# Kernel tuning notes

Hardware: AMD Instinct MI355X
Metric: run time of the kernel (lower is better)

The kernel has to match this reference:

```python
import jax, jax.numpy as jnp
import numpy as np

B, T, C, H = 2, 2048, 1024, 16
D = C // H
NEG = -1e9


def setup_inputs() -> dict:
    key = jax.random.key(0)
    ks = jax.random.split(key, 16)
    s = C ** -0.5
    hidden_states = jax.random.normal(ks[0], (B, T, C), dtype=jnp.float32)
    causal = jnp.tril(jnp.ones((T, T), dtype=bool))
    attention_mask = jnp.where(causal, 0.0, NEG).astype(jnp.float32)[None, None]
    p = lambda k, sh: jax.random.normal(k, sh, dtype=jnp.float32) * s
    return {
        "hidden_states": hidden_states,
        "attention_mask": attention_mask,
        "Wq": p(ks[1], (C, C)), "bq": jnp.zeros((C,), jnp.float32),
        "Wk": p(ks[2], (C, C)), "bk": jnp.zeros((C,), jnp.float32),
        "Wv": p(ks[3], (C, C)), "bv": jnp.zeros((C,), jnp.float32),
        "Wo": p(ks[4], (C, C)), "bo": jnp.zeros((C,), jnp.float32),
        "Wr1": p(ks[5], (C, C)), "br1": jnp.zeros((C,), jnp.float32),
        "Wr2": p(ks[6], (C, 3)), "br2": jnp.zeros((3,), jnp.float32),
    }


def reference(hidden_states, attention_mask, Wq, bq, Wk, bk, Wv, bv, Wo, bo, Wr1, br1, Wr2, br2):
    b, t, c = hidden_states.shape
    scale = D ** -0.5
    q = (hidden_states @ Wq + bq).reshape(b, t, H, D)
    k = (hidden_states @ Wk + bk).reshape(b, t, H, D)
    v = (hidden_states @ Wv + bv).reshape(b, t, H, D)
    # dead-end routing MLP (gate_logits computed but unused in the original)
    gate_logits = jnp.tanh(hidden_states @ Wr1 + br1) @ Wr2 + br2
    lambdas = jax.nn.softmax(gate_logits, axis=-1)  # noqa: F841 (unused, faithful)
    # explicit (unfused) attention: [B,H,T,T] scores materialized
    scores = jnp.einsum("bqhd,bkhd->bhqk", q, k) * scale + attention_mask
    probs = jax.nn.softmax(scores, axis=-1)
    ctx = jnp.einsum("bhqk,bkhd->bqhd", probs, v).reshape(b, t, c)
    return ctx @ Wo + bo
```

## Files before the change

### kernel.cpp

```cpp
#include <hip/hip_runtime.h>
#include <hip/hip_fp16.h>
#include <math.h>

#define BDIM 2
#define TDIM 2048
#define CDIM 1024
#define HDIM 16
#define DDIM 64

typedef _Float16 f16x8 __attribute__((ext_vector_type(8)));
typedef float f32x4 __attribute__((ext_vector_type(4)));

#define GLL16(gsrc, ldst)                                                      \
  __builtin_amdgcn_global_load_lds(                                            \
      (const __attribute__((address_space(1))) unsigned int*)(gsrc),           \
      (__attribute__((address_space(3))) unsigned int*)(ldst), 16, 0, 0)

#define SWZ(row) ((((row)&7) ^ (((row) >> 3) & 7)) << 4)

__global__ __launch_bounds__(256) void cvt_f16(const float* __restrict__ in,
                                               __half* __restrict__ out,
                                               int n8) {
  int i = blockIdx.x * blockDim.x + threadIdx.x;
  if (i >= n8) return;
  const float4* p = (const float4*)in + (size_t)i * 2;
  float4 a = p[0], b = p[1];
  __half2* o = (__half2*)out + (size_t)i * 4;
  o[0] = __floats2half2_rn(a.x, a.y);
  o[1] = __floats2half2_rn(a.z, a.w);
  o[2] = __floats2half2_rn(b.x, b.y);
  o[3] = __floats2half2_rn(b.z, b.w);
}

__global__ __launch_bounds__(256) void transpose_cvt(
    const float* __restrict__ w0, const float* __restrict__ w1,
    const float* __restrict__ w2, const float* __restrict__ w3,
    __half* __restrict__ o0, __half* __restrict__ o1, __half* __restrict__ o2,
    __half* __restrict__ o3) {
  const float* src;
  __half* dst;
  switch (blockIdx.z) {
    case 0: src = w0; dst = o0; break;
    case 1: src = w1; dst = o1; break;
    case 2: src = w2; dst = o2; break;
    default: src = w3; dst = o3; break;
  }
  __shared__ float t[32][33];
  const int tx = threadIdx.x & 31, ty = threadIdx.x >> 5;
  const int k0 = blockIdx.y * 32, n0 = blockIdx.x * 32;
#pragma unroll
  for (int j = 0; j < 4; ++j)
    t[ty + j * 8][tx] = src[(size_t)(k0 + ty + j * 8) * CDIM + n0 + tx];
  __syncthreads();
#pragma unroll
  for (int j = 0; j < 4; ++j)
    dst[(size_t)(n0 + ty + j * 8) * CDIM + k0 + tx] =
        __float2half(t[tx][ty + j * 8]);
}

template <int NMAT, int OUT16>
__global__ __launch_bounds__(256) void gemm_f16_bt(
    const __half* __restrict__ A, const __half* __restrict__ Bt,
    const float* __restrict__ bias0, const float* __restrict__ bias1,
    const float* __restrict__ bias2, float* __restrict__ outf,
    __half* __restrict__ outh, int M, int K) {
  __shared__ _Float16 As[2][128][32];
  __shared__ _Float16 Bs[2][128][32];
  const int tid = threadIdx.x;
  const int wid = tid >> 6, lane = tid & 63;
  const int m0 = blockIdx.y * 128, n0 = blockIdx.x * 128;
  const int wr = (wid >> 1) * 64, wc = (wid & 1) * 64;
  const int srow = lane >> 2;
  const int scol = (lane & 3) * 8;

  const __half* asrc = A + (size_t)(m0 + wid * 32 + srow) * K + scol;
  const __half* bsrc = Bt + (size_t)(n0 + wid * 32 + srow) * K + scol;

  f32x4 acc[4][4] = {};
  const int NT = K / 32;

  GLL16(asrc, &As[0][wid * 32][0]);
  GLL16(asrc + 16 * K, &As[0][wid * 32 + 16][0]);
  GLL16(bsrc, &Bs[0][wid * 32][0]);
  GLL16(bsrc + 16 * K, &Bs[0][wid * 32 + 16][0]);
  __syncthreads();

  for (int t = 0; t < NT; ++t) {
    const int cur = t & 1;
    if (t + 1 < NT) {
      const int k0 = (t + 1) * 32;
      GLL16(asrc + k0, &As[cur ^ 1][wid * 32][0]);
      GLL16(asrc + k0 + 16 * K, &As[cur ^ 1][wid * 32 + 16][0]);
      GLL16(bsrc + k0, &Bs[cur ^ 1][wid * 32][0]);
      GLL16(bsrc + k0 + 16 * K, &Bs[cur ^ 1][wid * 32 + 16][0]);
    }
    f16x8 a[4], b[4];
#pragma unroll
    for (int m = 0; m < 4; ++m)
      a[m] =
          *(const f16x8*)&As[cur][wr + m * 16 + (lane & 15)][(lane >> 4) * 8];
#pragma unroll
    for (int n = 0; n < 4; ++n)
      b[n] =
          *(const f16x8*)&Bs[cur][wc + n * 16 + (lane & 15)][(lane >> 4) * 8];
#pragma unroll
    for (int m = 0; m < 4; ++m)
#pragma unroll
      for (int n = 0; n < 4; ++n)
        acc[m][n] = __builtin_amdgcn_mfma_f32_16x16x32_f16(a[m], b[n],
                                                           acc[m][n], 0, 0, 0);
    __syncthreads();
  }

  const float* bias = bias0;
  size_t obase = 0;
  int ncol0 = n0;
  if (NMAT == 3) {
    const int mat = n0 >> 10;
    bias = (mat == 0) ? bias0 : (mat == 1) ? bias1 : bias2;
    obase = (size_t)mat * ((size_t)M * CDIM);
    ncol0 = n0 & 1023;
  }
#pragma unroll
  for (int m = 0; m < 4; ++m)
#pragma unroll
    for (int n = 0; n < 4; ++n) {
      const int col = ncol0 + wc + n * 16 + (lane & 15);
      const float bb = bias[col];
#pragma unroll
      for (int j = 0; j < 4; ++j) {
        const int row = m0 + wr + m * 16 + (lane >> 4) * 4 + j;
        if (OUT16)
          outh[obase + (size_t)row * CDIM + col] =
              __float2half(acc[m][n][j] + bb);
        else
          outf[(size_t)row * CDIM + col] = acc[m][n][j] + bb;
      }
    }
}

__global__ __launch_bounds__(256) void attention_mfma(
    const __half* __restrict__ q, const __half* __restrict__ k,
    const __half* __restrict__ v, __half* __restrict__ ctx) {
  __shared__ _Float16 Kl[2][64][64];
  __shared__ _Float16 Vt[2][64][64];
  __shared__ _Float16 Pl[4][16][64];

  const int tid = threadIdx.x;
  const int wid = tid >> 6, lane = tid & 63;
  const int qt = (blockIdx.x + blockIdx.y) & 31;
  const int bh = blockIdx.y;
  const int b = bh >> 4, h = bh & 15;
  const int qbase = qt * 64;
  const int g = lane >> 4, r = lane & 15;

  const __half* qhead = q + ((size_t)b * TDIM) * CDIM + h * DDIM;
  const __half* khead = k + ((size_t)b * TDIM) * CDIM + h * DDIM;
  const __half* vhead = v + ((size_t)b * TDIM) * CDIM + h * DDIM;

  f16x8 qf[2];
  {
    const __half* qrow = qhead + (size_t)(qbase + wid * 16 + r) * CDIM;
    qf[0] = *(const f16x8*)(qrow + g * 8);
    qf[1] = *(const f16x8*)(qrow + g * 8 + 32);
  }

  const int vrow = tid >> 2, vcol = (tid & 3) * 16;
  const int kr8 = lane >> 3;
  const int c0 = wid * 2, c1 = wid * 2 + 1;
  const int kcol0 = (((lane & 7) ^ kr8 ^ c0) & 7) * 8;
  const int kcol1 = (((lane & 7) ^ kr8 ^ c1) & 7) * 8;

  f32x4 acc_c[4] = {};
  float mj[4] = {-3.0e38f, -3.0e38f, -3.0e38f, -3.0e38f};
  float lj[4] = {};

  const int nt = qt + 1;

  f16x8 va, vb;
  {
    const __half* vsrc = vhead + (size_t)vrow * CDIM + vcol;
    va = *(const f16x8*)(vsrc);
    vb = *(const f16x8*)(vsrc + 8);
    GLL16(khead + (size_t)(c0 * 8 + kr8) * CDIM + kcol0, &Kl[0][c0 * 8][0]);
    GLL16(khead + (size_t)(c1 * 8 + kr8) * CDIM + kcol1, &Kl[0][c1 * 8][0]);
  }
  asm volatile("s_waitcnt vmcnt(0)" ::: "memory");
  __builtin_amdgcn_sched_barrier(0);
  {
    char* vt0 = (char*)&Vt[0][0][0];
#pragma unroll
    for (int i = 0; i < 8; ++i) {
      const int d0 = vcol + i, d1 = vcol + 8 + i;
      *(_Float16*)(vt0 + d0 * 128 + ((vrow * 2) ^ SWZ(d0))) = va[i];
      *(_Float16*)(vt0 + d1 * 128 + ((vrow * 2) ^ SWZ(d1))) = vb[i];
    }
  }
  __syncthreads();

  for (int t = 0; t < nt; ++t) {
    const int cur = t & 1, nxt = cur ^ 1;
    if (t + 1 < nt) {
      const __half* vsrc =
          vhead + (size_t)((t + 1) * 64 + vrow) * CDIM + vcol;
      va = *(const f16x8*)(vsrc);
      vb = *(const f16x8*)(vsrc + 8);
      GLL16(khead + (size_t)((t + 1) * 64 + c0 * 8 + kr8) * CDIM + kcol0,
            &Kl[nxt][c0 * 8][0]);
      GLL16(khead + (size_t)((t + 1) * 64 + c1 * 8 + kr8) * CDIM + kcol1,
            &Kl[nxt][c1 * 8][0]);
    }

    f32x4 s[4] = {};
    const char* klb = (const char*)&Kl[cur][0][0];
#pragma unroll
    for (int kk = 0; kk < 2; ++kk) {
#pragma unroll
      for (int n = 0; n < 4; ++n) {
        const int kcol = n * 16 + r;
        f16x8 kf = *(const f16x8*)(klb + kcol * 128 +
                                   ((g * 16 + kk * 64) ^ SWZ(kcol)));
        s[n] =
            __builtin_amdgcn_mfma_f32_16x16x32_f16(qf[kk], kf, s[n], 0, 0, 0);
      }
    }

    if (t == qt) {
#pragma unroll
      for (int n = 0; n < 4; ++n) {
        const int kg = t * 64 + n * 16 + r;
#pragma unroll
        for (int j = 0; j < 4; ++j) {
          const int qg = qbase + wid * 16 + g * 4 + j;
          s[n][j] = (kg <= qg) ? s[n][j] * 0.125f : -3.0e38f;
        }
      }
    } else {
#pragma unroll
      for (int n = 0; n < 4; ++n)
#pragma unroll
        for (int j = 0; j < 4; ++j) s[n][j] *= 0.125f;
    }

    float pj[4][4];
#pragma unroll
    for (int j = 0; j < 4; ++j) {
      float mx = fmaxf(fmaxf(s[0][j], s[1][j]), fmaxf(s[2][j], s[3][j]));
      mx = fmaxf(mx, __shfl_xor(mx, 1));
      mx = fmaxf(mx, __shfl_xor(mx, 2));
      mx = fmaxf(mx, __shfl_xor(mx, 4));
      mx = fmaxf(mx, __shfl_xor(mx, 8));
      const float mnew = fmaxf(mj[j], mx);
      const float corr = __expf(mj[j] - mnew);
      float sum = 0.f;
#pragma unroll
      for (int n = 0; n < 4; ++n) {
        pj[n][j] = __expf(s[n][j] - mnew);
        sum += pj[n][j];
      }
      sum += __shfl_xor(sum, 1);
      sum += __shfl_xor(sum, 2);
      sum += __shfl_xor(sum, 4);
      sum += __shfl_xor(sum, 8);
      lj[j] = lj[j] * corr + sum;
      mj[j] = mnew;
#pragma unroll
      for (int n = 0; n < 4; ++n) acc_c[n][j] *= corr;
    }

    char* pb = (char*)&Pl[wid][0][0];
#pragma unroll
    for (int n = 0; n < 4; ++n)
#pragma unroll
      for (int j = 0; j < 4; ++j) {
        const int qw = g * 4 + j, kcol = n * 16 + r;
        *(_Float16*)(pb + qw * 128 + ((kcol * 2) ^ SWZ(qw))) =
            (_Float16)pj[n][j];
      }

    const char* vtb = (const char*)&Vt[cur][0][0];
#pragma unroll
    for (int kk = 0; kk < 2; ++kk) {
      f16x8 pa =
          *(const f16x8*)(pb + r * 128 + ((g * 16 + kk * 64) ^ SWZ(r)));
#pragma unroll
      for (int n = 0; n < 4; ++n) {
        const int d = n * 16 + r;
        f16x8 vf =
            *(const f16x8*)(vtb + d * 128 + ((g * 16 + kk * 64) ^ SWZ(d)));
        acc_c[n] =
            __builtin_amdgcn_mfma_f32_16x16x32_f16(pa, vf, acc_c[n], 0, 0, 0);
      }
    }

    if (t + 1 < nt) {
      asm volatile("s_waitcnt vmcnt(0)" ::: "memory");
      __builtin_amdgcn_sched_barrier(0);
      char* vtn = (char*)&Vt[nxt][0][0];
#pragma unroll
      for (int i = 0; i < 8; ++i) {
        const int d0 = vcol + i, d1 = vcol + 8 + i;
        *(_Float16*)(vtn + d0 * 128 + ((vrow * 2) ^ SWZ(d0))) = va[i];
        *(_Float16*)(vtn + d1 * 128 + ((vrow * 2) ^ SWZ(d1))) = vb[i];
      }
    }
    __syncthreads();
  }

#pragma unroll
  for (int j = 0; j < 4; ++j) {
    const float inv = 1.0f / lj[j];
    const int qg = qbase + wid * 16 + g * 4 + j;
    __half* orow = ctx + ((size_t)(b * TDIM + qg)) * CDIM + h * DDIM;
#pragma unroll
    for (int n = 0; n < 4; ++n)
      orow[n * 16 + r] = __float2half(acc_c[n][j] * inv);
  }
}

extern "C" void kernel_launch(void* const* d_in, const int* in_sizes, int n_in,
                              void* d_out, int out_size, void* d_ws,
                              size_t ws_size, hipStream_t stream) {
  const float* hs = (const float*)d_in[0];
  const float* Wq = (const float*)d_in[2];
  const float* bq = (const float*)d_in[3];
  const float* Wk = (const float*)d_in[4];
  const float* bk = (const float*)d_in[5];
  const float* Wv = (const float*)d_in[6];
  const float* bv = (const float*)d_in[7];
  const float* Wo = (const float*)d_in[8];
  const float* bo = (const float*)d_in[9];
  float* out = (float*)d_out;

  const size_t NTOK = (size_t)BDIM * TDIM;
  const size_t NELEM = NTOK * CDIM;

  __half* q16 = (__half*)d_ws;
  __half* k16 = q16 + NELEM;
  __half* v16 = k16 + NELEM;
  __half* hs16 = v16 + NELEM;
  __half* ctx16 = hs16 + NELEM;
  __half* wqt = ctx16 + NELEM;
  __half* wkt = wqt + (size_t)CDIM * CDIM;
  __half* wvt = wkt + (size_t)CDIM * CDIM;
  __half* wot = wvt + (size_t)CDIM * CDIM;

  cvt_f16<<<dim3((NELEM / 8 + 255) / 256), dim3(256), 0, stream>>>(
      hs, hs16, (int)(NELEM / 8));
  transpose_cvt<<<dim3(32, 32, 4), dim3(256), 0, stream>>>(
      Wq, Wk, Wv, Wo, wqt, wkt, wvt, wot);

  dim3 gblk(256);
  gemm_f16_bt<3, 1><<<dim3(24, 32), gblk, 0, stream>>>(
      hs16, wqt, bq, bk, bv, nullptr, q16, (int)NTOK, CDIM);

  attention_mfma<<<dim3(TDIM / 64, BDIM * HDIM), dim3(256), 0, stream>>>(
      q16, k16, v16, ctx16);

  gemm_f16_bt<1, 0><<<dim3(8, 32), gblk, 0, stream>>>(
      ctx16, wot, bo, bo, bo, out, nullptr, (int)NTOK, CDIM);
}
```

Before: 292.9 us.

## Transpose attention MFMA layout so each lane owns one query row

Swaps the MFMA operand order for QK^T and PV so the accumulator holds S^T and O^T. Each lane then owns a single query row, which cuts the per-row softmax bookkeeping to one max/sum pair with two cross-lane shuffles. P is written to LDS and the output to global memory as packed 4-half vectors instead of scalar halfs. It also folds log2e into the scale to use exp2f, and relaxes the wait before the V-to-LDS transpose to vmcnt(2), which needs the V loads to retire before the K global-to-LDS loads.

```diff
diff --git a/kernel.cpp b/kernel.cpp
--- a/kernel.cpp
+++ b/kernel.cpp
@@ -9,6 +9,7 @@
 #define DDIM 64
 
 typedef _Float16 f16x8 __attribute__((ext_vector_type(8)));
+typedef _Float16 f16x4 __attribute__((ext_vector_type(4)));
 typedef float f32x4 __attribute__((ext_vector_type(4)));
 
 #define GLL16(gsrc, ldst)                                                      \
@@ -17,6 +18,8 @@
       (__attribute__((address_space(3))) unsigned int*)(ldst), 16, 0, 0)
 
 #define SWZ(row) ((((row)&7) ^ (((row) >> 3) & 7)) << 4)
+
+#define SCALE_LOG2E 0.1803368801111204f
 
 __global__ __launch_bounds__(256) void cvt_f16(const float* __restrict__ in,
                                                __half* __restrict__ out,
@@ -171,9 +174,8 @@
   const int kcol0 = (((lane & 7) ^ kr8 ^ c0) & 7) * 8;
   const int kcol1 = (((lane & 7) ^ kr8 ^ c1) & 7) * 8;
 
-  f32x4 acc_c[4] = {};
-  float mj[4] = {-3.0e38f, -3.0e38f, -3.0e38f, -3.0e38f};
-  float lj[4] = {};
+  f32x4 accT[4] = {};
+  float m = -3.0e38f, l = 0.0f;
 
   const int nt = qt + 1;
 
@@ -201,8 +203,7 @@
   for (int t = 0; t < nt; ++t) {
     const int cur = t & 1, nxt = cur ^ 1;
     if (t + 1 < nt) {
-      const __half* vsrc =
-          vhead + (size_t)((t + 1) * 64 + vrow) * CDIM + vcol;
+      const __half* vsrc = vhead + (size_t)((t + 1) * 64 + vrow) * CDIM + vcol;
       va = *(const f16x8*)(vsrc);
       vb = *(const f16x8*)(vsrc + 8);
       GLL16(khead + (size_t)((t + 1) * 64 + c0 * 8 + kr8) * CDIM + kcol0,
@@ -211,72 +212,70 @@
             &Kl[nxt][c1 * 8][0]);
     }
 
-    f32x4 s[4] = {};
+    f32x4 sT[4] = {};
     const char* klb = (const char*)&Kl[cur][0][0];
 #pragma unroll
     for (int kk = 0; kk < 2; ++kk) {
 #pragma unroll
-      for (int n = 0; n < 4; ++n) {
-        const int kcol = n * 16 + r;
-        f16x8 kf = *(const f16x8*)(klb + kcol * 128 +
-                                   ((g * 16 + kk * 64) ^ SWZ(kcol)));
-        s[n] =
-            __builtin_amdgcn_mfma_f32_16x16x32_f16(qf[kk], kf, s[n], 0, 0, 0);
-      }
-    }
-
+      for (int kb = 0; kb < 4; ++kb) {
+        const int krow = kb * 16 + r;
+        f16x8 kf = *(const f16x8*)(klb + krow * 128 +
+                                   ((g * 16 + kk * 64) ^ SWZ(krow)));
+        sT[kb] =
+            __builtin_amdgcn_mfma_f32_16x16x32_f16(kf, qf[kk], sT[kb], 0, 0, 0);
+      }
+    }
+
+    const int qg = qbase + wid * 16 + r;
     if (t == qt) {
 #pragma unroll
-      for (int n = 0; n < 4; ++n) {
-        const int kg = t * 64 + n * 16 + r;
-#pragma unroll
-        for (int j = 0; j < 4; ++j) {
-          const int qg = qbase + wid * 16 + g * 4 + j;
-          s[n][j] = (kg <= qg) ? s[n][j] * 0.125f : -3.0e38f;
-        }
+      for (int kb = 0; kb < 4; ++kb) {
+        const int kg = t * 64 + kb * 16 + g * 4;
+#pragma unroll
+        for (int j = 0; j < 4; ++j)
+          sT[kb][j] =
+              (kg + j <= qg) ? sT[kb][j] * SCALE_LOG2E : -3.0e38f;
       }
     } else {
 #pragma unroll
-      for (int n = 0; n < 4; ++n)
-#pragma unroll
-        for (int j = 0; j < 4; ++j) s[n][j] *= 0.125f;
-    }
-
-    float pj[4][4];
-#pragma unroll
-    for (int j = 0; j < 4; ++j) {
-      float mx = fmaxf(fmaxf(s[0][j], s[1][j]), fmaxf(s[2][j], s[3][j]));
-      mx = fmaxf(mx, __shfl_xor(mx, 1));
-      mx = fmaxf(mx, __shfl_xor(mx, 2));
-      mx = fmaxf(mx, __shfl_xor(mx, 4));
-      mx = fmaxf(mx, __shfl_xor(mx, 8));
-      const float mnew = fmaxf(mj[j], mx);
-      const float corr = __expf(mj[j] - mnew);
-      float sum = 0.f;
-#pragma unroll
-      for (int n = 0; n < 4; ++n) {
-        pj[n][j] = __expf(s[n][j] - mnew);
-        sum += pj[n][j];
-      }
-      sum += __shfl_xor(sum, 1);
-      sum += __shfl_xor(sum, 2);
-      sum += __shfl_xor(sum, 4);
-      sum += __shfl_xor(sum, 8);
-      lj[j] = lj[j] * corr + sum;
-      mj[j] = mnew;
-#pragma unroll
-      for (int n = 0; n < 4; ++n) acc_c[n][j] *= corr;
-    }
+      for (int kb = 0; kb < 4; ++kb)
+#pragma unroll
+        for (int j = 0; j < 4; ++j) sT[kb][j] *= SCALE_LOG2E;
+    }
+
+    float mx = sT[0][0];
+#pragma unroll
+    for (int kb = 0; kb < 4; ++kb)
+#pragma unroll
+      for (int j = 0; j < 4; ++j) mx = fmaxf(mx, sT[kb][j]);
+    mx = fmaxf(mx, __shfl_xor(mx, 16));
+    mx = fmaxf(mx, __shfl_xor(mx, 32));
+    const float mnew = fmaxf(m, mx);
+    const float corr = exp2f(m - mnew);
+    float psum = 0.f;
+    float pv[4][4];
+#pragma unroll
+    for (int kb = 0; kb < 4; ++kb)
+#pragma unroll
+      for (int j = 0; j < 4; ++j) {
+        pv[kb][j] = exp2f(sT[kb][j] - mnew);
+        psum += pv[kb][j];
+      }
+    psum += __shfl_xor(psum, 16);
+    psum += __shfl_xor(psum, 32);
+    l = l * corr + psum;
+    m = mnew;
+#pragma unroll
+    for (int n = 0; n < 4; ++n) accT[n] *= corr;
 
     char* pb = (char*)&Pl[wid][0][0];
 #pragma unroll
-    for (int n = 0; n < 4; ++n)
-#pragma unroll
-      for (int j = 0; j < 4; ++j) {
-        const int qw = g * 4 + j, kcol = n * 16 + r;
-        *(_Float16*)(pb + qw * 128 + ((kcol * 2) ^ SWZ(qw))) =
-            (_Float16)pj[n][j];
-      }
+    for (int kb = 0; kb < 4; ++kb) {
+      f16x4 pq;
+#pragma unroll
+      for (int j = 0; j < 4; ++j) pq[j] = (_Float16)pv[kb][j];
+      *(f16x4*)(pb + r * 128 + ((kb * 32 + g * 8) ^ SWZ(r))) = pq;
+    }
 
     const char* vtb = (const char*)&Vt[cur][0][0];
 #pragma unroll
@@ -285,16 +284,16 @@
           *(const f16x8*)(pb + r * 128 + ((g * 16 + kk * 64) ^ SWZ(r)));
 #pragma unroll
       for (int n = 0; n < 4; ++n) {
-        const int d = n * 16 + r;
+        const int vd = n * 16 + r;
         f16x8 vf =
-            *(const f16x8*)(vtb + d * 128 + ((g * 16 + kk * 64) ^ SWZ(d)));
-        acc_c[n] =
-            __builtin_amdgcn_mfma_f32_16x16x32_f16(pa, vf, acc_c[n], 0, 0, 0);
+            *(const f16x8*)(vtb + vd * 128 + ((g * 16 + kk * 64) ^ SWZ(vd)));
+        accT[n] =
+            __builtin_amdgcn_mfma_f32_16x16x32_f16(vf, pa, accT[n], 0, 0, 0);
       }
     }
 
     if (t + 1 < nt) {
-      asm volatile("s_waitcnt vmcnt(0)" ::: "memory");
+      asm volatile("s_waitcnt vmcnt(2)" ::: "memory");
       __builtin_amdgcn_sched_barrier(0);
       char* vtn = (char*)&Vt[nxt][0][0];
 #pragma unroll
@@ -307,14 +306,15 @@
     __syncthreads();
   }
 
-#pragma unroll
-  for (int j = 0; j < 4; ++j) {
-    const float inv = 1.0f / lj[j];
-    const int qg = qbase + wid * 16 + g * 4 + j;
-    __half* orow = ctx + ((size_t)(b * TDIM + qg)) * CDIM + h * DDIM;
-#pragma unroll
-    for (int n = 0; n < 4; ++n)
-      orow[n * 16 + r] = __float2half(acc_c[n][j] * inv);
+  const float inv = 1.0f / l;
+  const int qg = qbase + wid * 16 + r;
+  __half* orow = ctx + ((size_t)(b * TDIM + qg)) * CDIM + h * DDIM;
+#pragma unroll
+  for (int n = 0; n < 4; ++n) {
+    f16x4 ov;
+#pragma unroll
+    for (int j = 0; j < 4; ++j) ov[j] = (_Float16)(accT[n][j] * inv);
+    *(f16x4*)(orow + n * 16 + g * 4) = ov;
   }
 }
 
```

Result: faster. 258.1 us (-11.9%).
